# Kernel optimization log

Measured on AMD Instinct MI355X. Metric: run time of the kernel, lower is better.

## Reference

```python
import jax, jax.numpy as jnp
import numpy as np

B, S, D, F, E, K = 4, 2048, 512, 2048, 8, 2


def setup_inputs() -> dict:
    key = jax.random.key(0)
    kx, kg, kw, kv, k2 = jax.random.split(key, 5)
    scale = 0.02
    return {
        "x": jax.random.normal(kx, (B, S, D), dtype=jnp.float32),
        "Wg": jax.random.normal(kg, (D, E), dtype=jnp.float32) * scale,
        "W": jax.random.normal(kw, (E, D, F), dtype=jnp.float32) * scale,
        "V": jax.random.normal(kv, (E, D, F), dtype=jnp.float32) * scale,
        "W2": jax.random.normal(k2, (E, F, D), dtype=jnp.float32) * scale,
    }


def reference(x, Wg, W, V, W2):
    # Gating: top-k over expert logits, softmax over the selected k logits.
    gate_logits = jnp.einsum("bsd,de->bse", x, Wg)                 # [B,S,E]
    topv, topi = jax.lax.top_k(gate_logits, K)                      # [B,S,K]
    w = jax.nn.softmax(topv, axis=-1)                               # [B,S,K]
    # Dense per-token combine weights: gw[b,s,e] = sum_k w[b,s,k]*[topi[b,s,k]==e]
    gw = jnp.sum(w[..., None] * jax.nn.one_hot(topi, E, dtype=x.dtype), axis=-2)  # [B,S,E]

    y = jnp.zeros_like(x)
    n_experts = W.shape[0]
    for e in range(n_experts):  # fixed small loop over experts
        h = jax.nn.silu(jnp.einsum("bsd,df->bsf", x, W[e])) * jnp.einsum("bsd,df->bsf", x, V[e])
        y = y + gw[..., e:e + 1] * jnp.einsum("bsf,fd->bsd", h, W2[e])
    return y
```

## Files before the change

kernel.cpp:

```cpp
#include <hip/hip_runtime.h>
#include <hip/hip_bf16.h>
#include <stdint.h>

#define TT 8192
#define DD 512
#define FF 2048
#define EE 8
#define MAXT 136

typedef __attribute__((ext_vector_type(8))) short bf16x8;
typedef __attribute__((ext_vector_type(4))) float f32x4;

static __device__ __forceinline__ unsigned short f2b(float f) {
  union { __hip_bfloat16 b; unsigned short u; } cv;
  cv.b = __float2bfloat16(f);
  return cv.u;
}

static __device__ __forceinline__ void gload16(const void* g, void* l) {
  __builtin_amdgcn_global_load_lds(
      (const __attribute__((address_space(1))) unsigned int*)g,
      (__attribute__((address_space(3))) unsigned int*)l, 16, 0, 0);
}

__launch_bounds__(256)
__global__ void k_prep(const float* __restrict__ x, const float* __restrict__ Wg,
                       unsigned short* __restrict__ xb, float* __restrict__ y,
                       int* __restrict__ te, float* __restrict__ tw) {
  int wid = threadIdx.x >> 6, lane = threadIdx.x & 63;
  int t = blockIdx.x * 4 + wid;
  const float* xr = x + (size_t)t * DD;
  unsigned short* xbr = xb + (size_t)t * DD;
  float* yr = y + (size_t)t * DD;
  int d0 = lane * 8;

  float4 v0 = *(const float4*)(xr + d0);
  float4 v1 = *(const float4*)(xr + d0 + 4);
  ushort4 o0, o1;
  o0.x = f2b(v0.x); o0.y = f2b(v0.y); o0.z = f2b(v0.z); o0.w = f2b(v0.w);
  o1.x = f2b(v1.x); o1.y = f2b(v1.y); o1.z = f2b(v1.z); o1.w = f2b(v1.w);
  *(ushort4*)(xbr + d0) = o0;
  *(ushort4*)(xbr + d0 + 4) = o1;
  float4 z4 = make_float4(0.f, 0.f, 0.f, 0.f);
  *(float4*)(yr + d0) = z4;
  *(float4*)(yr + d0 + 4) = z4;

  float xv[8] = {v0.x, v0.y, v0.z, v0.w, v1.x, v1.y, v1.z, v1.w};
  float acc[EE];
#pragma unroll
  for (int e = 0; e < EE; e++) acc[e] = 0.f;
#pragma unroll
  for (int j = 0; j < 8; j++) {
    const float* wg = Wg + (size_t)(d0 + j) * EE;
    float4 a = *(const float4*)wg;
    float4 b = *(const float4*)(wg + 4);
    acc[0] += xv[j] * a.x; acc[1] += xv[j] * a.y; acc[2] += xv[j] * a.z; acc[3] += xv[j] * a.w;
    acc[4] += xv[j] * b.x; acc[5] += xv[j] * b.y; acc[6] += xv[j] * b.z; acc[7] += xv[j] * b.w;
  }
#pragma unroll
  for (int e = 0; e < EE; e++)
    for (int o = 32; o; o >>= 1) acc[e] += __shfl_xor(acc[e], o);
  if (lane == 0) {
    int e1 = 0; float v1m = acc[0];
#pragma unroll
    for (int e = 1; e < EE; e++) if (acc[e] > v1m) { v1m = acc[e]; e1 = e; }
    int e2 = -1; float v2m = -INFINITY;
#pragma unroll
    for (int e = 0; e < EE; e++) if (e != e1 && acc[e] > v2m) { v2m = acc[e]; e2 = e; }
    float ex = __expf(v2m - v1m);
    float w1 = 1.f / (1.f + ex);
    float w2 = ex / (1.f + ex);
    te[t * 2] = e1; te[t * 2 + 1] = e2;
    tw[t * 2] = w1; tw[t * 2 + 1] = w2;
  }
}

__global__ void k_tcvt_all(const float* __restrict__ W, const float* __restrict__ V,
                           const float* __restrict__ W2, unsigned short* __restrict__ Wt,
                           unsigned short* __restrict__ Vt, unsigned short* __restrict__ W2t) {
  __shared__ float tile[32][33];
  int z = blockIdx.y;
  const float* src; unsigned short* dst; int N, nbx;
  if (z < 16) {
    int e = z & 7;
    size_t base = (size_t)e * DD * FF;
    src = (z < 8 ? W : V) + base;
    dst = (z < 8 ? Wt : Vt) + base;
    N = FF; nbx = FF / 32;
  } else {
    int e = z - 16;
    size_t base = (size_t)e * DD * FF;
    src = W2 + base; dst = W2t + base;
    N = DD; nbx = DD / 32;
  }
  int M = (z < 16) ? DD : FF;
  int bx = blockIdx.x;
  int cb = (bx % nbx) * 32, rb = (bx / nbx) * 32;
  int tx = threadIdx.x, ty = threadIdx.y;
#pragma unroll
  for (int i = 0; i < 4; i++)
    tile[ty + i * 8][tx] = src[(size_t)(rb + ty + i * 8) * N + cb + tx];
  __syncthreads();
#pragma unroll
  for (int i = 0; i < 4; i++)
    dst[(size_t)(cb + ty + i * 8) * M + rb + tx] = f2b(tile[tx][ty + i * 8]);
}

__launch_bounds__(1024)
__global__ void k_route(const int* __restrict__ te, const float* __restrict__ tw,
                        int* __restrict__ ctrl, int* __restrict__ perm,
                        float* __restrict__ pw, int* __restrict__ tileE,
                        int* __restrict__ tileRow) {
  __shared__ int wsum[17][EE];
  __shared__ int ebase[EE];
  int tid = threadIdx.x;
  int lane = tid & 63, wid = tid >> 6;
  int myte[16]; float mytw[16];
  int c[EE];
#pragma unroll
  for (int e = 0; e < EE; e++) c[e] = 0;
  int s0 = tid * 16;
#pragma unroll
  for (int j = 0; j < 16; j++) {
    myte[j] = te[s0 + j];
    mytw[j] = tw[s0 + j];
#pragma unroll
    for (int e = 0; e < EE; e++) if (myte[j] == e) c[e]++;
  }
  int incl[EE];
#pragma unroll
  for (int e = 0; e < EE; e++) incl[e] = c[e];
  for (int off = 1; off < 64; off <<= 1) {
#pragma unroll
    for (int e = 0; e < EE; e++) {
      int v = __shfl_up(incl[e], off);
      if (lane >= off) incl[e] += v;
    }
  }
  if (lane == 63)
#pragma unroll
    for (int e = 0; e < EE; e++) wsum[wid][e] = incl[e];
  __syncthreads();
  if (tid < EE) {
    int s = 0;
    for (int w = 0; w < 16; w++) { int v = wsum[w][tid]; wsum[w][tid] = s; s += v; }
    wsum[16][tid] = s;
  }
  __syncthreads();
  if (tid == 0) {
    int s = 0, nt = 0;
    for (int e = 0; e < EE; e++) {
      int cnt = wsum[16][e];
      ebase[e] = s; ctrl[8 + e] = s; ctrl[e] = cnt;
      for (int i = 0; i < cnt; i += 128) { tileE[nt] = e; tileRow[nt] = s + i; nt++; }
      s += cnt;
    }
    ctrl[16] = s; ctrl[17] = nt;
  }
  __syncthreads();
#pragma unroll
  for (int e = 0; e < EE; e++) {
    int p = ebase[e] + wsum[wid][e] + incl[e] - c[e];
#pragma unroll
    for (int j = 0; j < 16; j++) {
      if (myte[j] == e) {
        perm[p] = (s0 + j) >> 1;
        pw[p] = mytw[j];
        p++;
      }
    }
  }
}

__launch_bounds__(256)
__global__ void k_ffn1(const unsigned short* __restrict__ xb,
                       const unsigned short* __restrict__ Wt,
                       const unsigned short* __restrict__ Vt,
                       const int* __restrict__ perm, const float* __restrict__ pw,
                       const int* __restrict__ ctrl, const int* __restrict__ tileE,
                       const int* __restrict__ tileRow,
                       unsigned short* __restrict__ h) {
  int ti = blockIdx.y;
  if (ti >= ctrl[17]) return;
  int e = tileE[ti];
  int row0 = tileRow[ti];
  int last = ctrl[8 + e] + ctrl[e] - 1;
  int f0 = blockIdx.x * 64;

  __shared__ __align__(16) short As[2][128 * 32];
  __shared__ __align__(16) short Bs[2][128 * 32];

  int tid = threadIdx.x;
  int lane = tid & 63, wid = tid >> 6;

  int ar1 = row0 + (tid >> 2); if (ar1 > last) ar1 = last;
  int ar2 = row0 + (tid >> 2) + 64; if (ar2 > last) ar2 = last;
  const unsigned short* agp1 = xb + (size_t)perm[ar1] * DD + (tid & 3) * 8;
  const unsigned short* agp2 = xb + (size_t)perm[ar2] * DD + (tid & 3) * 8;
  const unsigned short* wgp = Wt + ((size_t)e * FF + f0 + (tid >> 2)) * DD + (tid & 3) * 8;
  const unsigned short* vgp = Vt + ((size_t)e * FF + f0 + (tid >> 2)) * DD + (tid & 3) * 8;

#define STAGE1(buf, k0) do { \
    gload16(agp1 + (k0), &As[buf][tid * 8]); \
    gload16(agp2 + (k0), &As[buf][(tid + 256) * 8]); \
    gload16(wgp + (k0), &Bs[buf][tid * 8]); \
    gload16(vgp + (k0), &Bs[buf][(tid + 256) * 8]); \
  } while (0)

  f32x4 zz = {0.f, 0.f, 0.f, 0.f};
  f32x4 accw[2][4], accv[2][4];
#pragma unroll
  for (int m = 0; m < 2; m++)
#pragma unroll
    for (int n = 0; n < 4; n++) { accw[m][n] = zz; accv[m][n] = zz; }

  int lrow = lane & 15, kb = (lane >> 4) * 8;
  int a0off = (wid * 32 + lrow) * 32 + kb;

#define COMP1(buf) do { \
    bf16x8 a0 = *(bf16x8*)&As[buf][a0off]; \
    bf16x8 a1 = *(bf16x8*)&As[buf][a0off + 16 * 32]; \
    _Pragma("unroll") \
    for (int n = 0; n < 4; n++) { \
      bf16x8 bw = *(bf16x8*)&Bs[buf][(n * 16 + lrow) * 32 + kb]; \
      bf16x8 bv = *(bf16x8*)&Bs[buf][(64 + n * 16 + lrow) * 32 + kb]; \
      accw[0][n] = __builtin_amdgcn_mfma_f32_16x16x32_bf16(a0, bw, accw[0][n], 0, 0, 0); \
      accw[1][n] = __builtin_amdgcn_mfma_f32_16x16x32_bf16(a1, bw, accw[1][n], 0, 0, 0); \
      accv[0][n] = __builtin_amdgcn_mfma_f32_16x16x32_bf16(a0, bv, accv[0][n], 0, 0, 0); \
      accv[1][n] = __builtin_amdgcn_mfma_f32_16x16x32_bf16(a1, bv, accv[1][n], 0, 0, 0); \
    } \
  } while (0)

  STAGE1(0, 0);
  __syncthreads();
#pragma unroll 1
  for (int ks = 0; ks < 16; ks += 2) {
    if (ks + 1 < 16) STAGE1(1, (ks + 1) * 32);
    COMP1(0);
    __syncthreads();
    if (ks + 2 < 16) STAGE1(0, (ks + 2) * 32);
    COMP1(1);
    __syncthreads();
  }
#undef STAGE1
#undef COMP1

#pragma unroll
  for (int m = 0; m < 2; m++) {
    int rbase = row0 + wid * 32 + m * 16 + (lane >> 4) * 4;
#pragma unroll
    for (int reg = 0; reg < 4; reg++) {
      int r = rbase + reg;
      if (r > last) continue;
      float pwv = pw[r];
      size_t hrow = (size_t)r * FF;
#pragma unroll
      for (int n = 0; n < 4; n++) {
        float a = accw[m][n][reg];
        float b = accv[m][n][reg];
        float hv = a / (1.f + __expf(-a)) * b * pwv;
        h[hrow + f0 + n * 16 + lrow] = f2b(hv);
      }
    }
  }
}

__launch_bounds__(256)
__global__ void k_ffn2(const unsigned short* __restrict__ h,
                       const unsigned short* __restrict__ W2t,
                       const int* __restrict__ perm, const int* __restrict__ ctrl,
                       const int* __restrict__ tileE, const int* __restrict__ tileRow,
                       float* __restrict__ y) {
  int ti = blockIdx.y;
  if (ti >= ctrl[17]) return;
  int e = tileE[ti];
  int row0 = tileRow[ti];
  int last = ctrl[8 + e] + ctrl[e] - 1;
  int d0 = blockIdx.x * 128;

  __shared__ __align__(16) short As[2][128 * 32];
  __shared__ __align__(16) short Bs[2][128 * 32];

  int tid = threadIdx.x;
  int lane = tid & 63, wid = tid >> 6;
  int wm = (wid >> 1) * 64, wn = (wid & 1) * 64;

  int ar1 = row0 + (tid >> 2); if (ar1 > last) ar1 = last;
  int ar2 = row0 + (tid >> 2) + 64; if (ar2 > last) ar2 = last;
  const unsigned short* agp1 = h + (size_t)ar1 * FF + (tid & 3) * 8;
  const unsigned short* agp2 = h + (size_t)ar2 * FF + (tid & 3) * 8;
  const unsigned short* bgp1 = W2t + ((size_t)e * DD + d0 + (tid >> 2)) * FF + (tid & 3) * 8;
  const unsigned short* bgp2 = bgp1 + (size_t)64 * FF;

#define STAGE2(buf, k0) do { \
    gload16(agp1 + (k0), &As[buf][tid * 8]); \
    gload16(agp2 + (k0), &As[buf][(tid + 256) * 8]); \
    gload16(bgp1 + (k0), &Bs[buf][tid * 8]); \
    gload16(bgp2 + (k0), &Bs[buf][(tid + 256) * 8]); \
  } while (0)

  f32x4 zz = {0.f, 0.f, 0.f, 0.f};
  f32x4 acc[4][4];
#pragma unroll
  for (int m = 0; m < 4; m++)
#pragma unroll
    for (int n = 0; n < 4; n++) acc[m][n] = zz;

  int lrow = lane & 15, kb = (lane >> 4) * 8;

#define COMP2(buf) do { \
    bf16x8 a[4], b[4]; \
    _Pragma("unroll") \
    for (int m = 0; m < 4; m++) a[m] = *(bf16x8*)&As[buf][(wm + m * 16 + lrow) * 32 + kb]; \
    _Pragma("unroll") \
    for (int n = 0; n < 4; n++) b[n] = *(bf16x8*)&Bs[buf][(wn + n * 16 + lrow) * 32 + kb]; \
    _Pragma("unroll") \
    for (int m = 0; m < 4; m++) \
      _Pragma("unroll") \
      for (int n = 0; n < 4; n++) \
        acc[m][n] = __builtin_amdgcn_mfma_f32_16x16x32_bf16(a[m], b[n], acc[m][n], 0, 0, 0); \
  } while (0)

  STAGE2(0, 0);
  __syncthreads();
#pragma unroll 1
  for (int ks = 0; ks < 64; ks += 2) {
    if (ks + 1 < 64) STAGE2(1, (ks + 1) * 32);
    COMP2(0);
    __syncthreads();
    if (ks + 2 < 64) STAGE2(0, (ks + 2) * 32);
    COMP2(1);
    __syncthreads();
  }
#undef STAGE2
#undef COMP2

#pragma unroll
  for (int m = 0; m < 4; m++) {
    int rbase = row0 + wm + m * 16 + (lane >> 4) * 4;
#pragma unroll
    for (int reg = 0; reg < 4; reg++) {
      int r = rbase + reg;
      if (r > last) continue;
      int t = perm[r];
      size_t yrow = (size_t)t * DD;
#pragma unroll
      for (int n = 0; n < 4; n++)
        atomicAdd(&y[yrow + d0 + wn + n * 16 + lrow], acc[m][n][reg]);
    }
  }
}

extern "C" void kernel_launch(void* const* d_in, const int* in_sizes, int n_in,
                              void* d_out, int out_size, void* d_ws, size_t ws_size,
                              hipStream_t stream) {
  const float* x  = (const float*)d_in[0];
  const float* Wg = (const float*)d_in[1];
  const float* W  = (const float*)d_in[2];
  const float* V  = (const float*)d_in[3];
  const float* W2 = (const float*)d_in[4];
  float* y = (float*)d_out;

  char* ws = (char*)d_ws;
  size_t off = 0;
  auto alloc = [&](size_t n) -> char* {
    char* p = ws + off;
    off += (n + 255) & ~(size_t)255;
    return p;
  };
  unsigned short* xb  = (unsigned short*)alloc((size_t)TT * DD * 2);
  unsigned short* Wt  = (unsigned short*)alloc((size_t)EE * DD * FF * 2);
  unsigned short* Vt  = (unsigned short*)alloc((size_t)EE * DD * FF * 2);
  unsigned short* W2t = (unsigned short*)alloc((size_t)EE * DD * FF * 2);
  unsigned short* h   = (unsigned short*)alloc((size_t)TT * 2 * FF * 2);
  int*   perm = (int*)alloc(TT * 2 * 4);
  float* pw   = (float*)alloc(TT * 2 * 4);
  int*   te   = (int*)alloc(TT * 2 * 4);
  float* tw   = (float*)alloc(TT * 2 * 4);
  int*   ctrl = (int*)alloc(256);
  int*   tileE   = (int*)alloc(MAXT * 4);
  int*   tileRow = (int*)alloc(MAXT * 4);
  if (off > ws_size) return;

  k_prep<<<TT / 4, 256, 0, stream>>>(x, Wg, xb, y, te, tw);
  k_tcvt_all<<<dim3(1024, 24), dim3(32, 8), 0, stream>>>(W, V, W2, Wt, Vt, W2t);
  k_route<<<1, 1024, 0, stream>>>(te, tw, ctrl, perm, pw, tileE, tileRow);
  k_ffn1<<<dim3(FF / 64, MAXT), 256, 0, stream>>>(xb, Wt, Vt, perm, pw, ctrl, tileE, tileRow, h);
  k_ffn2<<<dim3(DD / 128, MAXT), 256, 0, stream>>>(h, W2t, perm, ctrl, tileE, tileRow, y);
}
```

Measured before the change: 255.9 us.

## Triple-buffer FFN GEMM tiles with vmcnt waits and XOR-swizzled LDS layout

```diff
diff --git a/kernel.cpp b/kernel.cpp
--- a/kernel.cpp
+++ b/kernel.cpp
@@ -22,6 +22,10 @@
       (const __attribute__((address_space(1))) unsigned int*)g,
       (__attribute__((address_space(3))) unsigned int*)l, 16, 0, 0);
 }
+
+#define VMCNT(n) asm volatile("s_waitcnt vmcnt(" #n ")" ::: "memory")
+#define SBAR() do { __builtin_amdgcn_sched_barrier(0); __builtin_amdgcn_s_barrier(); \
+                    __builtin_amdgcn_sched_barrier(0); } while (0)
 
 __launch_bounds__(256)
 __global__ void k_prep(const float* __restrict__ x, const float* __restrict__ Wg,
@@ -187,24 +191,27 @@
   int last = ctrl[8 + e] + ctrl[e] - 1;
   int f0 = blockIdx.x * 64;
 
-  __shared__ __align__(16) short As[2][128 * 32];
-  __shared__ __align__(16) short Bs[2][128 * 32];
+  __shared__ __align__(16) short As[3][128 * 32];
+  __shared__ __align__(16) short Bs[3][128 * 32];
 
   int tid = threadIdx.x;
   int lane = tid & 63, wid = tid >> 6;
 
+  int sl = (((tid & 3) ^ ((tid >> 3) & 3))) * 8;
+
   int ar1 = row0 + (tid >> 2); if (ar1 > last) ar1 = last;
   int ar2 = row0 + (tid >> 2) + 64; if (ar2 > last) ar2 = last;
-  const unsigned short* agp1 = xb + (size_t)perm[ar1] * DD + (tid & 3) * 8;
-  const unsigned short* agp2 = xb + (size_t)perm[ar2] * DD + (tid & 3) * 8;
-  const unsigned short* wgp = Wt + ((size_t)e * FF + f0 + (tid >> 2)) * DD + (tid & 3) * 8;
-  const unsigned short* vgp = Vt + ((size_t)e * FF + f0 + (tid >> 2)) * DD + (tid & 3) * 8;
-
-#define STAGE1(buf, k0) do { \
-    gload16(agp1 + (k0), &As[buf][tid * 8]); \
-    gload16(agp2 + (k0), &As[buf][(tid + 256) * 8]); \
-    gload16(wgp + (k0), &Bs[buf][tid * 8]); \
-    gload16(vgp + (k0), &Bs[buf][(tid + 256) * 8]); \
+  const unsigned short* agp1 = xb + (size_t)perm[ar1] * DD + sl;
+  const unsigned short* agp2 = xb + (size_t)perm[ar2] * DD + sl;
+  const unsigned short* wgp = Wt + ((size_t)e * FF + f0 + (tid >> 2)) * DD + sl;
+  const unsigned short* vgp = Vt + ((size_t)e * FF + f0 + (tid >> 2)) * DD + sl;
+
+#define STAGE1(buf, know) do { \
+    int k0_ = (know) * 32; \
+    gload16(agp1 + k0_, &As[buf][tid * 8]); \
+    gload16(agp2 + k0_, &As[buf][(tid + 256) * 8]); \
+    gload16(wgp + k0_, &Bs[buf][tid * 8]); \
+    gload16(vgp + k0_, &Bs[buf][(tid + 256) * 8]); \
   } while (0)
 
   f32x4 zz = {0.f, 0.f, 0.f, 0.f};
@@ -214,16 +221,17 @@
 #pragma unroll
     for (int n = 0; n < 4; n++) { accw[m][n] = zz; accv[m][n] = zz; }
 
-  int lrow = lane & 15, kb = (lane >> 4) * 8;
-  int a0off = (wid * 32 + lrow) * 32 + kb;
+  int lrow = lane & 15;
+  int jx = (((lane >> 4) ^ ((lane >> 1) & 3))) * 8;
+  int a0off = (wid * 32 + lrow) * 32 + jx;
 
 #define COMP1(buf) do { \
     bf16x8 a0 = *(bf16x8*)&As[buf][a0off]; \
     bf16x8 a1 = *(bf16x8*)&As[buf][a0off + 16 * 32]; \
     _Pragma("unroll") \
     for (int n = 0; n < 4; n++) { \
-      bf16x8 bw = *(bf16x8*)&Bs[buf][(n * 16 + lrow) * 32 + kb]; \
-      bf16x8 bv = *(bf16x8*)&Bs[buf][(64 + n * 16 + lrow) * 32 + kb]; \
+      bf16x8 bw = *(bf16x8*)&Bs[buf][(n * 16 + lrow) * 32 + jx]; \
+      bf16x8 bv = *(bf16x8*)&Bs[buf][(64 + n * 16 + lrow) * 32 + jx]; \
       accw[0][n] = __builtin_amdgcn_mfma_f32_16x16x32_bf16(a0, bw, accw[0][n], 0, 0, 0); \
       accw[1][n] = __builtin_amdgcn_mfma_f32_16x16x32_bf16(a1, bw, accw[1][n], 0, 0, 0); \
       accv[0][n] = __builtin_amdgcn_mfma_f32_16x16x32_bf16(a0, bv, accv[0][n], 0, 0, 0); \
@@ -231,17 +239,25 @@
     } \
   } while (0)
 
-  STAGE1(0, 0);
-  __syncthreads();
+#define ITER1(buf, know) do { \
+    VMCNT(8); SBAR(); \
+    COMP1(buf); \
+    SBAR(); \
+    STAGE1(buf, know); \
+  } while (0)
+
+  STAGE1(0, 0); STAGE1(1, 1); STAGE1(2, 2);
 #pragma unroll 1
-  for (int ks = 0; ks < 16; ks += 2) {
-    if (ks + 1 < 16) STAGE1(1, (ks + 1) * 32);
-    COMP1(0);
-    __syncthreads();
-    if (ks + 2 < 16) STAGE1(0, (ks + 2) * 32);
-    COMP1(1);
-    __syncthreads();
-  }
+  for (int kt = 0; kt < 4; kt++) {
+    ITER1(0, kt * 3 + 3);
+    ITER1(1, kt * 3 + 4);
+    ITER1(2, kt * 3 + 5);
+  }
+  ITER1(0, 15);
+  VMCNT(8); SBAR(); COMP1(1);
+  VMCNT(4); SBAR(); COMP1(2);
+  VMCNT(0); SBAR(); COMP1(0);
+#undef ITER1
 #undef STAGE1
 #undef COMP1
 
@@ -278,25 +294,28 @@
   int last = ctrl[8 + e] + ctrl[e] - 1;
   int d0 = blockIdx.x * 128;
 
-  __shared__ __align__(16) short As[2][128 * 32];
-  __shared__ __align__(16) short Bs[2][128 * 32];
+  __shared__ __align__(16) short As[3][128 * 32];
+  __shared__ __align__(16) short Bs[3][128 * 32];
 
   int tid = threadIdx.x;
   int lane = tid & 63, wid = tid >> 6;
   int wm = (wid >> 1) * 64, wn = (wid & 1) * 64;
 
+  int sl = (((tid & 3) ^ ((tid >> 3) & 3))) * 8;
+
   int ar1 = row0 + (tid >> 2); if (ar1 > last) ar1 = last;
   int ar2 = row0 + (tid >> 2) + 64; if (ar2 > last) ar2 = last;
-  const unsigned short* agp1 = h + (size_t)ar1 * FF + (tid & 3) * 8;
-  const unsigned short* agp2 = h + (size_t)ar2 * FF + (tid & 3) * 8;
-  const unsigned short* bgp1 = W2t + ((size_t)e * DD + d0 + (tid >> 2)) * FF + (tid & 3) * 8;
+  const unsigned short* agp1 = h + (size_t)ar1 * FF + sl;
+  const unsigned short* agp2 = h + (size_t)ar2 * FF + sl;
+  const unsigned short* bgp1 = W2t + ((size_t)e * DD + d0 + (tid >> 2)) * FF + sl;
   const unsigned short* bgp2 = bgp1 + (size_t)64 * FF;
 
-#define STAGE2(buf, k0) do { \
-    gload16(agp1 + (k0), &As[buf][tid * 8]); \
-    gload16(agp2 + (k0), &As[buf][(tid + 256) * 8]); \
-    gload16(bgp1 + (k0), &Bs[buf][tid * 8]); \
-    gload16(bgp2 + (k0), &Bs[buf][(tid + 256) * 8]); \
+#define STAGE2(buf, know) do { \
+    int k0_ = (know) * 32; \
+    gload16(agp1 + k0_, &As[buf][tid * 8]); \
+    gload16(agp2 + k0_, &As[buf][(tid + 256) * 8]); \
+    gload16(bgp1 + k0_, &Bs[buf][tid * 8]); \
+    gload16(bgp2 + k0_, &Bs[buf][(tid + 256) * 8]); \
   } while (0)
 
   f32x4 zz = {0.f, 0.f, 0.f, 0.f};
@@ -306,14 +325,15 @@
 #pragma unroll
     for (int n = 0; n < 4; n++) acc[m][n] = zz;
 
-  int lrow = lane & 15, kb = (lane >> 4) * 8;
+  int lrow = lane & 15;
+  int jx = (((lane >> 4) ^ ((lane >> 1) & 3))) * 8;
 
 #define COMP2(buf) do { \
     bf16x8 a[4], b[4]; \
     _Pragma("unroll") \
-    for (int m = 0; m < 4; m++) a[m] = *(bf16x8*)&As[buf][(wm + m * 16 + lrow) * 32 + kb]; \
+    for (int m = 0; m < 4; m++) a[m] = *(bf16x8*)&As[buf][(wm + m * 16 + lrow) * 32 + jx]; \
     _Pragma("unroll") \
-    for (int n = 0; n < 4; n++) b[n] = *(bf16x8*)&Bs[buf][(wn + n * 16 + lrow) * 32 + kb]; \
+    for (int n = 0; n < 4; n++) b[n] = *(bf16x8*)&Bs[buf][(wn + n * 16 + lrow) * 32 + jx]; \
     _Pragma("unroll") \
     for (int m = 0; m < 4; m++) \
       _Pragma("unroll") \
@@ -321,17 +341,25 @@
         acc[m][n] = __builtin_amdgcn_mfma_f32_16x16x32_bf16(a[m], b[n], acc[m][n], 0, 0, 0); \
   } while (0)
 
-  STAGE2(0, 0);
-  __syncthreads();
+#define ITER2(buf, know) do { \
+    VMCNT(8); SBAR(); \
+    COMP2(buf); \
+    SBAR(); \
+    STAGE2(buf, know); \
+  } while (0)
+
+  STAGE2(0, 0); STAGE2(1, 1); STAGE2(2, 2);
 #pragma unroll 1
-  for (int ks = 0; ks < 64; ks += 2) {
-    if (ks + 1 < 64) STAGE2(1, (ks + 1) * 32);
-    COMP2(0);
-    __syncthreads();
-    if (ks + 2 < 64) STAGE2(0, (ks + 2) * 32);
-    COMP2(1);
-    __syncthreads();
-  }
+  for (int kt = 0; kt < 20; kt++) {
+    ITER2(0, kt * 3 + 3);
+    ITER2(1, kt * 3 + 4);
+    ITER2(2, kt * 3 + 5);
+  }
+  ITER2(0, 63);
+  VMCNT(8); SBAR(); COMP2(1);
+  VMCNT(4); SBAR(); COMP2(2);
+  VMCNT(0); SBAR(); COMP2(0);
+#undef ITER2
 #undef STAGE2
 #undef COMP2
 
```

Result: slower. 280.4 us (+9.6%).

## Replace ffn2 atomic scatter with per-slot stores plus gather, swizzle LDS reads

Applied to the files above, without the earlier changes.

```diff
diff --git a/kernel.cpp b/kernel.cpp
--- a/kernel.cpp
+++ b/kernel.cpp
@@ -25,13 +25,12 @@
 
 __launch_bounds__(256)
 __global__ void k_prep(const float* __restrict__ x, const float* __restrict__ Wg,
-                       unsigned short* __restrict__ xb, float* __restrict__ y,
+                       unsigned short* __restrict__ xb,
                        int* __restrict__ te, float* __restrict__ tw) {
   int wid = threadIdx.x >> 6, lane = threadIdx.x & 63;
   int t = blockIdx.x * 4 + wid;
   const float* xr = x + (size_t)t * DD;
   unsigned short* xbr = xb + (size_t)t * DD;
-  float* yr = y + (size_t)t * DD;
   int d0 = lane * 8;
 
   float4 v0 = *(const float4*)(xr + d0);
@@ -41,9 +40,6 @@
   o1.x = f2b(v1.x); o1.y = f2b(v1.y); o1.z = f2b(v1.z); o1.w = f2b(v1.w);
   *(ushort4*)(xbr + d0) = o0;
   *(ushort4*)(xbr + d0 + 4) = o1;
-  float4 z4 = make_float4(0.f, 0.f, 0.f, 0.f);
-  *(float4*)(yr + d0) = z4;
-  *(float4*)(yr + d0 + 4) = z4;
 
   float xv[8] = {v0.x, v0.y, v0.z, v0.w, v1.x, v1.y, v1.z, v1.w};
   float acc[EE];
@@ -110,7 +106,7 @@
 __global__ void k_route(const int* __restrict__ te, const float* __restrict__ tw,
                         int* __restrict__ ctrl, int* __restrict__ perm,
                         float* __restrict__ pw, int* __restrict__ tileE,
-                        int* __restrict__ tileRow) {
+                        int* __restrict__ tileRow, int* __restrict__ inv) {
   __shared__ int wsum[17][EE];
   __shared__ int ebase[EE];
   int tid = threadIdx.x;
@@ -166,6 +162,7 @@
       if (myte[j] == e) {
         perm[p] = (s0 + j) >> 1;
         pw[p] = mytw[j];
+        inv[s0 + j] = p;
         p++;
       }
     }
@@ -193,12 +190,14 @@
   int tid = threadIdx.x;
   int lane = tid & 63, wid = tid >> 6;
 
+  int sl = (((tid & 3) ^ ((tid >> 3) & 3))) * 8;
+
   int ar1 = row0 + (tid >> 2); if (ar1 > last) ar1 = last;
   int ar2 = row0 + (tid >> 2) + 64; if (ar2 > last) ar2 = last;
-  const unsigned short* agp1 = xb + (size_t)perm[ar1] * DD + (tid & 3) * 8;
-  const unsigned short* agp2 = xb + (size_t)perm[ar2] * DD + (tid & 3) * 8;
-  const unsigned short* wgp = Wt + ((size_t)e * FF + f0 + (tid >> 2)) * DD + (tid & 3) * 8;
-  const unsigned short* vgp = Vt + ((size_t)e * FF + f0 + (tid >> 2)) * DD + (tid & 3) * 8;
+  const unsigned short* agp1 = xb + (size_t)perm[ar1] * DD + sl;
+  const unsigned short* agp2 = xb + (size_t)perm[ar2] * DD + sl;
+  const unsigned short* wgp = Wt + ((size_t)e * FF + f0 + (tid >> 2)) * DD + sl;
+  const unsigned short* vgp = Vt + ((size_t)e * FF + f0 + (tid >> 2)) * DD + sl;
 
 #define STAGE1(buf, k0) do { \
     gload16(agp1 + (k0), &As[buf][tid * 8]); \
@@ -214,16 +213,17 @@
 #pragma unroll
     for (int n = 0; n < 4; n++) { accw[m][n] = zz; accv[m][n] = zz; }
 
-  int lrow = lane & 15, kb = (lane >> 4) * 8;
-  int a0off = (wid * 32 + lrow) * 32 + kb;
+  int lrow = lane & 15;
+  int jx = (((lane >> 4) ^ ((lane >> 1) & 3))) * 8;
+  int a0off = (wid * 32 + lrow) * 32 + jx;
 
 #define COMP1(buf) do { \
     bf16x8 a0 = *(bf16x8*)&As[buf][a0off]; \
     bf16x8 a1 = *(bf16x8*)&As[buf][a0off + 16 * 32]; \
     _Pragma("unroll") \
     for (int n = 0; n < 4; n++) { \
-      bf16x8 bw = *(bf16x8*)&Bs[buf][(n * 16 + lrow) * 32 + kb]; \
-      bf16x8 bv = *(bf16x8*)&Bs[buf][(64 + n * 16 + lrow) * 32 + kb]; \
+      bf16x8 bw = *(bf16x8*)&Bs[buf][(n * 16 + lrow) * 32 + jx]; \
+      bf16x8 bv = *(bf16x8*)&Bs[buf][(64 + n * 16 + lrow) * 32 + jx]; \
       accw[0][n] = __builtin_amdgcn_mfma_f32_16x16x32_bf16(a0, bw, accw[0][n], 0, 0, 0); \
       accw[1][n] = __builtin_amdgcn_mfma_f32_16x16x32_bf16(a1, bw, accw[1][n], 0, 0, 0); \
       accv[0][n] = __builtin_amdgcn_mfma_f32_16x16x32_bf16(a0, bv, accv[0][n], 0, 0, 0); \
@@ -268,9 +268,9 @@
 __launch_bounds__(256)
 __global__ void k_ffn2(const unsigned short* __restrict__ h,
                        const unsigned short* __restrict__ W2t,
-                       const int* __restrict__ perm, const int* __restrict__ ctrl,
+                       const int* __restrict__ ctrl,
                        const int* __restrict__ tileE, const int* __restrict__ tileRow,
-                       float* __restrict__ y) {
+                       float* __restrict__ yp) {
   int ti = blockIdx.y;
   if (ti >= ctrl[17]) return;
   int e = tileE[ti];
@@ -285,11 +285,13 @@
   int lane = tid & 63, wid = tid >> 6;
   int wm = (wid >> 1) * 64, wn = (wid & 1) * 64;
 
+  int sl = (((tid & 3) ^ ((tid >> 3) & 3))) * 8;
+
   int ar1 = row0 + (tid >> 2); if (ar1 > last) ar1 = last;
   int ar2 = row0 + (tid >> 2) + 64; if (ar2 > last) ar2 = last;
-  const unsigned short* agp1 = h + (size_t)ar1 * FF + (tid & 3) * 8;
-  const unsigned short* agp2 = h + (size_t)ar2 * FF + (tid & 3) * 8;
-  const unsigned short* bgp1 = W2t + ((size_t)e * DD + d0 + (tid >> 2)) * FF + (tid & 3) * 8;
+  const unsigned short* agp1 = h + (size_t)ar1 * FF + sl;
+  const unsigned short* agp2 = h + (size_t)ar2 * FF + sl;
+  const unsigned short* bgp1 = W2t + ((size_t)e * DD + d0 + (tid >> 2)) * FF + sl;
   const unsigned short* bgp2 = bgp1 + (size_t)64 * FF;
 
 #define STAGE2(buf, k0) do { \
@@ -306,14 +308,15 @@
 #pragma unroll
     for (int n = 0; n < 4; n++) acc[m][n] = zz;
 
-  int lrow = lane & 15, kb = (lane >> 4) * 8;
+  int lrow = lane & 15;
+  int jx = (((lane >> 4) ^ ((lane >> 1) & 3))) * 8;
 
 #define COMP2(buf) do { \
     bf16x8 a[4], b[4]; \
     _Pragma("unroll") \
-    for (int m = 0; m < 4; m++) a[m] = *(bf16x8*)&As[buf][(wm + m * 16 + lrow) * 32 + kb]; \
+    for (int m = 0; m < 4; m++) a[m] = *(bf16x8*)&As[buf][(wm + m * 16 + lrow) * 32 + jx]; \
     _Pragma("unroll") \
-    for (int n = 0; n < 4; n++) b[n] = *(bf16x8*)&Bs[buf][(wn + n * 16 + lrow) * 32 + kb]; \
+    for (int n = 0; n < 4; n++) b[n] = *(bf16x8*)&Bs[buf][(wn + n * 16 + lrow) * 32 + jx]; \
     _Pragma("unroll") \
     for (int m = 0; m < 4; m++) \
       _Pragma("unroll") \
@@ -342,13 +345,25 @@
     for (int reg = 0; reg < 4; reg++) {
       int r = rbase + reg;
       if (r > last) continue;
-      int t = perm[r];
-      size_t yrow = (size_t)t * DD;
+      float* ypr = yp + (size_t)r * DD + d0;
 #pragma unroll
       for (int n = 0; n < 4; n++)
-        atomicAdd(&y[yrow + d0 + wn + n * 16 + lrow], acc[m][n][reg]);
+        ypr[wn + n * 16 + lrow] = acc[m][n][reg];
     }
   }
+}
+
+__launch_bounds__(256)
+__global__ void k_gather(const float4* __restrict__ yp4, const int* __restrict__ inv,
+                         float4* __restrict__ y4) {
+  int i = blockIdx.x * 256 + threadIdx.x;
+  int t = i >> 7, c = i & 127;
+  int pa = inv[2 * t], pb = inv[2 * t + 1];
+  float4 a = yp4[(size_t)pa * 128 + c];
+  float4 b = yp4[(size_t)pb * 128 + c];
+  float4 o;
+  o.x = a.x + b.x; o.y = a.y + b.y; o.z = a.z + b.z; o.w = a.w + b.w;
+  y4[i] = o;
 }
 
 extern "C" void kernel_launch(void* const* d_in, const int* in_sizes, int n_in,
@@ -377,14 +392,18 @@
   float* pw   = (float*)alloc(TT * 2 * 4);
   int*   te   = (int*)alloc(TT * 2 * 4);
   float* tw   = (float*)alloc(TT * 2 * 4);
+  int*   inv  = (int*)alloc(TT * 2 * 4);
   int*   ctrl = (int*)alloc(256);
   int*   tileE   = (int*)alloc(MAXT * 4);
   int*   tileRow = (int*)alloc(MAXT * 4);
   if (off > ws_size) return;
 
-  k_prep<<<TT / 4, 256, 0, stream>>>(x, Wg, xb, y, te, tw);
+  float* yp = (float*)Wt;
+
+  k_prep<<<TT / 4, 256, 0, stream>>>(x, Wg, xb, te, tw);
   k_tcvt_all<<<dim3(1024, 24), dim3(32, 8), 0, stream>>>(W, V, W2, Wt, Vt, W2t);
-  k_route<<<1, 1024, 0, stream>>>(te, tw, ctrl, perm, pw, tileE, tileRow);
+  k_route<<<1, 1024, 0, stream>>>(te, tw, ctrl, perm, pw, tileE, tileRow, inv);
   k_ffn1<<<dim3(FF / 64, MAXT), 256, 0, stream>>>(xb, Wt, Vt, perm, pw, ctrl, tileE, tileRow, h);
-  k_ffn2<<<dim3(DD / 128, MAXT), 256, 0, stream>>>(h, W2t, perm, ctrl, tileE, tileRow, y);
-}
+  k_ffn2<<<dim3(DD / 128, MAXT), 256, 0, stream>>>(h, W2t, ctrl, tileE, tileRow, yp);
+  k_gather<<<TT * 128 / 256, 256, 0, stream>>>((const float4*)yp, inv, (float4*)y);
+}
```

New measurement: 252.4 us. No clear change (-1.4%).
